# Kernel optimization log

Measured on AMD Instinct MI355X. Metric: run time of the kernel, lower is better.

Reference implementation:

```python
import jax, jax.numpy as jnp
import numpy as np

D = 64            # number of devices (leaves hold D/8 each)
B = 65536         # batch of states
FEAT = 5 + 4 * D  # 261
HID = 128


def setup_inputs() -> dict:
    key = jax.random.key(0)
    ks = jax.random.split(key, 10)
    def nrm(k, shape, s=0.1):
        return jax.random.normal(k, shape, jnp.float32) * s
    return {
        "x": jax.random.normal(ks[0], (B, FEAT), jnp.float32),
        # gate params per depth d: 2^d nodes, weight dim 5 + 4*D/2^d
        "w0": nrm(ks[1], (1, 5 + 4 * D)),
        "b0": jnp.zeros((1,), jnp.float32),
        "w1": nrm(ks[2], (2, 5 + 4 * (D // 2))),
        "b1": jnp.zeros((2,), jnp.float32),
        "w2": nrm(ks[3], (4, 5 + 4 * (D // 4))),
        "b2": jnp.zeros((4,), jnp.float32),
        # leaf prob_dist (torch inits to zeros; random here for a non-trivial baseline)
        "leaf_probs": nrm(ks[4], (8, D // 8), 1.0),
        # critic MLP
        "Wc1": nrm(ks[5], (FEAT, HID)),
        "bc1": jnp.zeros((HID,), jnp.float32),
        "Wc2": nrm(ks[6], (HID, 1)),
        "bc2": jnp.zeros((1,), jnp.float32),
    }


def reference(x, w0, b0, w1, b1, w2, b2, leaf_probs, Wc1, bc1, Wc2, bc2):
    # Batched deterministic ClusterTree routing (exploration disabled).
    x5 = x[:, :5]                       # (B, 5) global features
    dev = x[:, 5:].reshape(B, D, 4)     # (B, D, 4) per-device features
    node = jnp.zeros((B,), jnp.int32)   # current node index at each depth
    cum = jnp.ones((B,), x.dtype)       # product of gate values along path
    for d, (wd, bd) in enumerate([(w0, b0), (w1, b1), (w2, b2)]):
        nd = D >> d                     # devices per node at this depth
        off = node * nd                 # contiguous-cluster start offset
        idx = off[:, None] + jnp.arange(nd)                     # (B, nd)
        dslice = jnp.take_along_axis(dev, idx[:, :, None], 1)   # (B, nd, 4)
        w = wd[node]                    # (B, 5 + 4*nd)
        gate = (jnp.sum(x5 * w[:, :5], -1)
                + jnp.sum(dslice.reshape(B, -1) * w[:, 5:], -1)
                + bd[node])
        val = jax.nn.sigmoid(gate)
        cum = cum * val                 # torch: val * child_output, recursively
        node = node * 2 + (val >= 0.5).astype(jnp.int32)
    p = cum[:, None] * leaf_probs[node]                 # (B, D//8)
    v = jax.nn.relu(x @ Wc1 + bc1) @ Wc2 + bc2          # (B, 1) critic
    return p, v
```

## Files before the change

### kernel.cpp

```cpp
#include <hip/hip_runtime.h>
#include <hip/hip_bf16.h>
#include <stdint.h>

#define NB    65536
#define FEATN 261
#define HIDN  128
#define NSTEP 17
#define SROW  296

#define ROWSF 64
#define NTHRF 256

typedef __attribute__((ext_vector_type(8)))  short bf16x8;
typedef __attribute__((ext_vector_type(16))) float f32x16;
typedef float f32x4u __attribute__((ext_vector_type(4), aligned(4)));

#define MFMA32(A, B, C) __builtin_amdgcn_mfma_f32_32x32x16_bf16(A, B, C, 0, 0, 0)

__device__ __forceinline__ uint16_t f2b(float v) {
    __hip_bfloat16 b = __float2bfloat16(v);
    return *reinterpret_cast<uint16_t*>(&b);
}

__global__ void prep_kernel(const float* __restrict__ Wc1,
                            uint16_t* __restrict__ wsB)
{
    int t = blockIdx.x * 256 + threadIdx.x;
    if (t < NSTEP * 4 * 64) {
        int p = t >> 6, l = t & 63;
        int s = p >> 2, nt = p & 3;
        int n = nt * 32 + (l & 31);
        int kb = 16 * s + 8 * (l >> 5);
        uint16_t hw[8];
        #pragma unroll
        for (int j = 0; j < 8; ++j) {
            int k = kb + j;
            float v = (k < FEATN) ? Wc1[(size_t)k * HIDN + n] : 0.f;
            hw[j] = f2b(v);
        }
        *reinterpret_cast<uint4*>(wsB + (size_t)p * 512 + l * 8) =
            *reinterpret_cast<uint4*>(hw);
    }
}

__global__ __launch_bounds__(NTHRF, 4) void fused_kernel(
    const float* __restrict__ x,
    const float* __restrict__ w0, const float* __restrict__ b0,
    const float* __restrict__ w1, const float* __restrict__ b1,
    const float* __restrict__ w2, const float* __restrict__ b2,
    const float* __restrict__ leaf,
    const uint16_t* __restrict__ wsB,
    const float* __restrict__ bc1, const float* __restrict__ Wc2,
    const float* __restrict__ bc2,
    float* __restrict__ out_p, float* __restrict__ out_v)
{
    __shared__ uint16_t Axs[ROWSF * SROW];
    __shared__ float bc1s[HIDN];
    __shared__ float wc2s[HIDN];
    __shared__ float vpart[ROWSF * 2];

    const int tid = threadIdx.x;
    const int rowBase = blockIdx.x * ROWSF;

    if (tid < HIDN) { bc1s[tid] = bc1[tid]; wc2s[tid] = Wc2[tid]; }
    if (tid < ROWSF) {
        uint16_t* rp = Axs + tid * SROW;
        rp[261] = 0;
        *reinterpret_cast<uint32_t*>(rp + 262) = 0u;
        uint4 z; z.x = z.y = z.z = z.w = 0u;
        *reinterpret_cast<uint4*>(rp + 264) = z;
        *reinterpret_cast<uint4*>(rp + 272) = z;
        *reinterpret_cast<uint4*>(rp + 280) = z;
        *reinterpret_cast<uint4*>(rp + 288) = z;
    }

    for (int idx = tid; idx < ROWSF * 66; idx += NTHRF) {
        int row = idx / 66;
        int seg = idx - row * 66;
        const float* src = x + (size_t)(rowBase + row) * FEATN + 4 * seg;
        uint16_t* dst = Axs + row * SROW + 4 * seg;
        if (seg < 65) {
            f32x4u v = *reinterpret_cast<const f32x4u*>(src);
            uint32_t p0 = (uint32_t)f2b(v[0]) | ((uint32_t)f2b(v[1]) << 16);
            uint32_t p1 = (uint32_t)f2b(v[2]) | ((uint32_t)f2b(v[3]) << 16);
            uint2 pk; pk.x = p0; pk.y = p1;
            *reinterpret_cast<uint2*>(dst) = pk;
        } else {
            dst[0] = f2b(src[0]);
        }
    }

    {
        const int s = tid & 15;
        const int g = tid >> 4;

        f32x4u w0q[4];
        #pragma unroll
        for (int j = 0; j < 4; ++j)
            w0q[j] = *reinterpret_cast<const f32x4u*>(w0 + 4 * s + 64 * j);
        const float w0t = (s < 5) ? w0[256 + s] : 0.f;

        f32x4u w1aq[2], w1bq[2];
        #pragma unroll
        for (int j = 0; j < 2; ++j) {
            w1aq[j] = *reinterpret_cast<const f32x4u*>(w1 + 5 + 8 * s + 4 * j);
            w1bq[j] = *reinterpret_cast<const f32x4u*>(w1 + 133 + 5 + 8 * s + 4 * j);
        }
        const float w1a5 = (s < 5) ? w1[s]       : 0.f;
        const float w1b5 = (s < 5) ? w1[133 + s] : 0.f;

        f32x4u w2q0 = *reinterpret_cast<const f32x4u*>(w2 +  0 * 69 + 5 + 4 * s);
        f32x4u w2q1 = *reinterpret_cast<const f32x4u*>(w2 +  1 * 69 + 5 + 4 * s);
        f32x4u w2q2 = *reinterpret_cast<const f32x4u*>(w2 +  2 * 69 + 5 + 4 * s);
        f32x4u w2q3 = *reinterpret_cast<const f32x4u*>(w2 +  3 * 69 + 5 + 4 * s);
        const float w25_0 = (s < 5) ? w2[0 * 69 + s] : 0.f;
        const float w25_1 = (s < 5) ? w2[1 * 69 + s] : 0.f;
        const float w25_2 = (s < 5) ? w2[2 * 69 + s] : 0.f;
        const float w25_3 = (s < 5) ? w2[3 * 69 + s] : 0.f;

        #pragma unroll 1
        for (int r4 = 0; r4 < 4; ++r4) {
            const int row = rowBase + r4 * 16 + g;
            const float* xr = x + (size_t)row * FEATN;

            f32x4u xq[4];
            #pragma unroll
            for (int j = 0; j < 4; ++j)
                xq[j] = *reinterpret_cast<const f32x4u*>(xr + 4 * s + 64 * j);
            const float xt  = (s < 5) ? xr[256 + s] : 0.f;
            const float xs5 = (s < 5) ? xr[s]       : 0.f;

            float part = xt * w0t;
            #pragma unroll
            for (int j = 0; j < 4; ++j)
                #pragma unroll
                for (int c = 0; c < 4; ++c)
                    part += xq[j][c] * w0q[j][c];
            part += __shfl_xor(part, 1);
            part += __shfl_xor(part, 2);
            part += __shfl_xor(part, 4);
            part += __shfl_xor(part, 8);
            float gate = part + b0[0];
            int node = (gate >= 0.f) ? 1 : 0;
            float cum = 1.f / (1.f + __expf(-gate));

            {
                const float* base = xr + 5 + 128 * node + 8 * s;
                f32x4u xw0 = *reinterpret_cast<const f32x4u*>(base);
                f32x4u xw1 = *reinterpret_cast<const f32x4u*>(base + 4);
                part = xs5 * (node ? w1b5 : w1a5);
                #pragma unroll
                for (int c = 0; c < 4; ++c) {
                    part += xw0[c] * (node ? w1bq[0][c] : w1aq[0][c]);
                    part += xw1[c] * (node ? w1bq[1][c] : w1aq[1][c]);
                }
                part += __shfl_xor(part, 1);
                part += __shfl_xor(part, 2);
                part += __shfl_xor(part, 4);
                part += __shfl_xor(part, 8);
                gate = part + b1[node];
                cum *= 1.f / (1.f + __expf(-gate));
                node = node * 2 + ((gate >= 0.f) ? 1 : 0);
            }
            {
                f32x4u xv2 = *reinterpret_cast<const f32x4u*>(xr + 5 + 64 * node + 4 * s);
                f32x4u t0 = (node & 1) ? w2q1 : w2q0;
                f32x4u t1 = (node & 1) ? w2q3 : w2q2;
                f32x4u wsel = (node & 2) ? t1 : t0;
                float w5a = (node & 1) ? w25_1 : w25_0;
                float w5b = (node & 1) ? w25_3 : w25_2;
                float w5sel = (node & 2) ? w5b : w5a;
                part = xs5 * w5sel;
                #pragma unroll
                for (int c = 0; c < 4; ++c) part += xv2[c] * wsel[c];
                part += __shfl_xor(part, 1);
                part += __shfl_xor(part, 2);
                part += __shfl_xor(part, 4);
                part += __shfl_xor(part, 8);
                gate = part + b2[node];
                cum *= 1.f / (1.f + __expf(-gate));
                node = node * 2 + ((gate >= 0.f) ? 1 : 0);
            }
            if (s < 8)
                out_p[(size_t)row * 8 + s] = cum * leaf[node * 8 + s];
        }
    }

    __syncthreads();

    const int lane = tid & 63;
    const int w    = tid >> 6;
    const int mt   = w >> 1;
    const int nh   = w & 1;

    const uint16_t* arow = Axs + (mt * 32 + (lane & 31)) * SROW + (lane >> 5) * 8;
    const uint16_t* bgl  = wsB + (size_t)(2 * nh) * 512 + lane * 8;

    f32x16 acc0 = {}, acc1 = {};
    #pragma unroll
    for (int ss = 0; ss < NSTEP; ++ss) {
        bf16x8 af  = *reinterpret_cast<const bf16x8*>(arow + ss * 16);
        bf16x8 bf0 = *reinterpret_cast<const bf16x8*>(bgl + (size_t)(ss * 4)     * 512);
        bf16x8 bf1 = *reinterpret_cast<const bf16x8*>(bgl + (size_t)(ss * 4 + 1) * 512);
        acc0 = MFMA32(af, bf0, acc0);
        acc1 = MFMA32(af, bf1, acc1);
    }

    {
        const int c = lane & 31;
        const int q = lane >> 5;
        const int n0 = 2 * nh * 32 + c;
        const int n1 = n0 + 32;
        const float bb0 = bc1s[n0], ww0 = wc2s[n0];
        const float bb1 = bc1s[n1], ww1 = wc2s[n1];

        float pv[16];
        #pragma unroll
        for (int reg = 0; reg < 16; ++reg) {
            float h0 = acc0[reg] + bb0; h0 = h0 > 0.f ? h0 : 0.f;
            float h1 = acc1[reg] + bb1; h1 = h1 > 0.f ? h1 : 0.f;
            float t = h0 * ww0 + h1 * ww1;
            t += __shfl_xor(t, 1);
            t += __shfl_xor(t, 2);
            t += __shfl_xor(t, 4);
            t += __shfl_xor(t, 8);
            t += __shfl_xor(t, 16);
            pv[reg] = t;
        }
        #pragma unroll
        for (int reg = 0; reg < 16; ++reg) {
            if (c == reg) {
                int row_local = (reg & 3) + 8 * (reg >> 2) + 4 * q;
                vpart[(mt * 32 + row_local) * 2 + nh] = pv[reg];
            }
        }
    }
    __syncthreads();
    if (tid < ROWSF)
        out_v[rowBase + tid] = vpart[tid * 2] + vpart[tid * 2 + 1] + bc2[0];
}

extern "C" void kernel_launch(void* const* d_in, const int* in_sizes, int n_in,
                              void* d_out, int out_size, void* d_ws, size_t ws_size,
                              hipStream_t stream) {
    const float* x    = (const float*)d_in[0];
    const float* w0   = (const float*)d_in[1];
    const float* b0   = (const float*)d_in[2];
    const float* w1   = (const float*)d_in[3];
    const float* b1   = (const float*)d_in[4];
    const float* w2   = (const float*)d_in[5];
    const float* b2   = (const float*)d_in[6];
    const float* leaf = (const float*)d_in[7];
    const float* Wc1  = (const float*)d_in[8];
    const float* bc1  = (const float*)d_in[9];
    const float* Wc2  = (const float*)d_in[10];
    const float* bc2  = (const float*)d_in[11];

    uint16_t* wsB = (uint16_t*)d_ws;

    float* out_p = (float*)d_out;
    float* out_v = out_p + (size_t)NB * 8;

    prep_kernel<<<17, 256, 0, stream>>>(Wc1, wsB);
    fused_kernel<<<NB / ROWSF, NTHRF, 0, stream>>>(
        x, w0, b0, w1, b1, w2, b2, leaf, wsB, bc1, Wc2, bc2, out_p, out_v);
}
```

Baseline: 147.0 us.

## Fuse x staging into routing loop and precompute all gate partials speculatively

The separate pass that loads x and converts it to bf16 in shared memory is removed; the routing loop now writes the bf16 row into shared memory from the x registers it already loaded, so x is read from global memory once instead of twice. The gate partial sums for every node at every depth are computed from that single load using rearranged weight registers. The data-dependent reloads of x at depths 1 and 2 are replaced by selecting among the precomputed partials. This removes dependent global loads from the routing chain, at the cost of extra FMAs and a few more weight registers.

Result: faster. 128.0 us, median of 2 (-12.9%).

```diff
diff --git a/kernel.cpp b/kernel.cpp
--- a/kernel.cpp
+++ b/kernel.cpp
@@ -21,6 +21,13 @@
     __hip_bfloat16 b = __float2bfloat16(v);
     return *reinterpret_cast<uint16_t*>(&b);
 }
+
+__device__ __forceinline__ float sigmoidf(float g) {
+    return 1.f / (1.f + __expf(-g));
+}
+
+#define RED16(v) do { v += __shfl_xor(v, 1); v += __shfl_xor(v, 2); \
+                      v += __shfl_xor(v, 4); v += __shfl_xor(v, 8); } while (0)
 
 __global__ void prep_kernel(const float* __restrict__ Wc1,
                             uint16_t* __restrict__ wsB)
@@ -74,116 +81,116 @@
         *reinterpret_cast<uint4*>(rp + 288) = z;
     }
 
-    for (int idx = tid; idx < ROWSF * 66; idx += NTHRF) {
-        int row = idx / 66;
-        int seg = idx - row * 66;
-        const float* src = x + (size_t)(rowBase + row) * FEATN + 4 * seg;
-        uint16_t* dst = Axs + row * SROW + 4 * seg;
-        if (seg < 65) {
-            f32x4u v = *reinterpret_cast<const f32x4u*>(src);
-            uint32_t p0 = (uint32_t)f2b(v[0]) | ((uint32_t)f2b(v[1]) << 16);
-            uint32_t p1 = (uint32_t)f2b(v[2]) | ((uint32_t)f2b(v[3]) << 16);
-            uint2 pk; pk.x = p0; pk.y = p1;
-            *reinterpret_cast<uint2*>(dst) = pk;
-        } else {
-            dst[0] = f2b(src[0]);
-        }
-    }
-
-    {
-        const int s = tid & 15;
-        const int g = tid >> 4;
-
-        f32x4u w0q[4];
+    const int s = tid & 15;
+    const int g = tid >> 4;
+
+    f32x4u w0q[4];
+    #pragma unroll
+    for (int j = 0; j < 4; ++j)
+        w0q[j] = *reinterpret_cast<const f32x4u*>(w0 + 64 * j + 4 * s);
+    const float w0t = (s < 5) ? w0[256 + s] : 0.f;
+
+    float w1v[4][4], w2v[4][4];
+    #pragma unroll
+    for (int j = 0; j < 4; ++j)
+        #pragma unroll
+        for (int c = 0; c < 4; ++c) {
+            int e = 64 * j + 4 * s + c;
+            w1v[j][c] = w1[(e < 133) ? e : e + 5];
+            int n2 = (e < 5) ? 0 : ((e - 5) >> 6);
+            w2v[j][c] = w2[e + 5 * n2];
+        }
+    const float w1t = (s < 5) ? w1[261 + s] : 0.f;
+    const float w2t = (s < 5) ? w2[271 + s] : 0.f;
+
+    const float xw1b  = (s < 5) ? w1[133 + s] : 0.f;
+    const float xw2_1 = (s < 5) ? w2[ 69 + s] : 0.f;
+    const float xw2_2 = (s < 5) ? w2[138 + s] : 0.f;
+    const float xw2_3 = (s < 5) ? w2[207 + s] : 0.f;
+
+    const float b0s  = b0[0];
+    const float b1s0 = b1[0], b1s1 = b1[1];
+    const float b2s0 = b2[0], b2s1 = b2[1], b2s2 = b2[2], b2s3 = b2[3];
+
+    #pragma unroll 1
+    for (int r4 = 0; r4 < 4; ++r4) {
+        const int rl  = r4 * 16 + g;
+        const int row = rowBase + rl;
+        const float* xr = x + (size_t)row * FEATN;
+
+        f32x4u xq[4];
         #pragma unroll
         for (int j = 0; j < 4; ++j)
-            w0q[j] = *reinterpret_cast<const f32x4u*>(w0 + 4 * s + 64 * j);
-        const float w0t = (s < 5) ? w0[256 + s] : 0.f;
-
-        f32x4u w1aq[2], w1bq[2];
-        #pragma unroll
-        for (int j = 0; j < 2; ++j) {
-            w1aq[j] = *reinterpret_cast<const f32x4u*>(w1 + 5 + 8 * s + 4 * j);
-            w1bq[j] = *reinterpret_cast<const f32x4u*>(w1 + 133 + 5 + 8 * s + 4 * j);
-        }
-        const float w1a5 = (s < 5) ? w1[s]       : 0.f;
-        const float w1b5 = (s < 5) ? w1[133 + s] : 0.f;
-
-        f32x4u w2q0 = *reinterpret_cast<const f32x4u*>(w2 +  0 * 69 + 5 + 4 * s);
-        f32x4u w2q1 = *reinterpret_cast<const f32x4u*>(w2 +  1 * 69 + 5 + 4 * s);
-        f32x4u w2q2 = *reinterpret_cast<const f32x4u*>(w2 +  2 * 69 + 5 + 4 * s);
-        f32x4u w2q3 = *reinterpret_cast<const f32x4u*>(w2 +  3 * 69 + 5 + 4 * s);
-        const float w25_0 = (s < 5) ? w2[0 * 69 + s] : 0.f;
-        const float w25_1 = (s < 5) ? w2[1 * 69 + s] : 0.f;
-        const float w25_2 = (s < 5) ? w2[2 * 69 + s] : 0.f;
-        const float w25_3 = (s < 5) ? w2[3 * 69 + s] : 0.f;
-
-        #pragma unroll 1
-        for (int r4 = 0; r4 < 4; ++r4) {
-            const int row = rowBase + r4 * 16 + g;
-            const float* xr = x + (size_t)row * FEATN;
-
-            f32x4u xq[4];
+            xq[j] = *reinterpret_cast<const f32x4u*>(xr + 64 * j + 4 * s);
+        const float xt  = (s < 5) ? xr[256 + s] : 0.f;
+        const float xs5 = (s < 5) ? xr[s]       : 0.f;
+
+        {
+            uint16_t* rp = Axs + rl * SROW;
             #pragma unroll
-            for (int j = 0; j < 4; ++j)
-                xq[j] = *reinterpret_cast<const f32x4u*>(xr + 4 * s + 64 * j);
-            const float xt  = (s < 5) ? xr[256 + s] : 0.f;
-            const float xs5 = (s < 5) ? xr[s]       : 0.f;
-
-            float part = xt * w0t;
+            for (int j = 0; j < 4; ++j) {
+                uint32_t p0w = (uint32_t)f2b(xq[j][0]) | ((uint32_t)f2b(xq[j][1]) << 16);
+                uint32_t p1w = (uint32_t)f2b(xq[j][2]) | ((uint32_t)f2b(xq[j][3]) << 16);
+                uint2 pk; pk.x = p0w; pk.y = p1w;
+                *reinterpret_cast<uint2*>(rp + 64 * j + 4 * s) = pk;
+            }
+            if (s < 5) rp[256 + s] = f2b(xt);
+        }
+
+        float p0 = 0.f, p1a = 0.f, p1b = 0.f;
+        float p2_0 = 0.f, p2_1 = 0.f, p2_2 = 0.f, p2_3 = 0.f;
+        #pragma unroll
+        for (int j = 0; j < 4; ++j)
             #pragma unroll
-            for (int j = 0; j < 4; ++j)
-                #pragma unroll
-                for (int c = 0; c < 4; ++c)
-                    part += xq[j][c] * w0q[j][c];
-            part += __shfl_xor(part, 1);
-            part += __shfl_xor(part, 2);
-            part += __shfl_xor(part, 4);
-            part += __shfl_xor(part, 8);
-            float gate = part + b0[0];
-            int node = (gate >= 0.f) ? 1 : 0;
-            float cum = 1.f / (1.f + __expf(-gate));
-
-            {
-                const float* base = xr + 5 + 128 * node + 8 * s;
-                f32x4u xw0 = *reinterpret_cast<const f32x4u*>(base);
-                f32x4u xw1 = *reinterpret_cast<const f32x4u*>(base + 4);
-                part = xs5 * (node ? w1b5 : w1a5);
-                #pragma unroll
-                for (int c = 0; c < 4; ++c) {
-                    part += xw0[c] * (node ? w1bq[0][c] : w1aq[0][c]);
-                    part += xw1[c] * (node ? w1bq[1][c] : w1aq[1][c]);
+            for (int c = 0; c < 4; ++c) {
+                const float xv = xq[j][c];
+                const bool lo = (4 * s + c) < 5;
+                p0 += xv * w0q[j][c];
+                const float t1 = xv * w1v[j][c];
+                const float t2 = xv * w2v[j][c];
+                if (j == 0) {
+                    p1a += t1;
+                    p2_0 += t2;
+                } else if (j == 1) {
+                    p1a += t1;
+                    p2_0 += lo ? t2 : 0.f;  p2_1 += lo ? 0.f : t2;
+                } else if (j == 2) {
+                    p1a += lo ? t1 : 0.f;   p1b += lo ? 0.f : t1;
+                    p2_1 += lo ? t2 : 0.f;  p2_2 += lo ? 0.f : t2;
+                } else {
+                    p1b += t1;
+                    p2_2 += lo ? t2 : 0.f;  p2_3 += lo ? 0.f : t2;
                 }
-                part += __shfl_xor(part, 1);
-                part += __shfl_xor(part, 2);
-                part += __shfl_xor(part, 4);
-                part += __shfl_xor(part, 8);
-                gate = part + b1[node];
-                cum *= 1.f / (1.f + __expf(-gate));
-                node = node * 2 + ((gate >= 0.f) ? 1 : 0);
             }
-            {
-                f32x4u xv2 = *reinterpret_cast<const f32x4u*>(xr + 5 + 64 * node + 4 * s);
-                f32x4u t0 = (node & 1) ? w2q1 : w2q0;
-                f32x4u t1 = (node & 1) ? w2q3 : w2q2;
-                f32x4u wsel = (node & 2) ? t1 : t0;
-                float w5a = (node & 1) ? w25_1 : w25_0;
-                float w5b = (node & 1) ? w25_3 : w25_2;
-                float w5sel = (node & 2) ? w5b : w5a;
-                part = xs5 * w5sel;
-                #pragma unroll
-                for (int c = 0; c < 4; ++c) part += xv2[c] * wsel[c];
-                part += __shfl_xor(part, 1);
-                part += __shfl_xor(part, 2);
-                part += __shfl_xor(part, 4);
-                part += __shfl_xor(part, 8);
-                gate = part + b2[node];
-                cum *= 1.f / (1.f + __expf(-gate));
-                node = node * 2 + ((gate >= 0.f) ? 1 : 0);
-            }
-            if (s < 8)
-                out_p[(size_t)row * 8 + s] = cum * leaf[node * 8 + s];
-        }
+        p0   += xt * w0t;
+        p1b  += xt * w1t;
+        p2_3 += xt * w2t;
+        p1b  += xs5 * xw1b;
+        p2_1 += xs5 * xw2_1;
+        p2_2 += xs5 * xw2_2;
+        p2_3 += xs5 * xw2_3;
+
+        RED16(p0);
+        const float gate0 = p0 + b0s;
+        int nn = (gate0 >= 0.f) ? 1 : 0;
+        float cum = sigmoidf(gate0);
+
+        float p1 = nn ? p1b : p1a;
+        RED16(p1);
+        const float gate1 = p1 + (nn ? b1s1 : b1s0);
+        nn = nn * 2 + ((gate1 >= 0.f) ? 1 : 0);
+        cum *= sigmoidf(gate1);
+
+        float p2 = (nn & 2) ? ((nn & 1) ? p2_3 : p2_2)
+                            : ((nn & 1) ? p2_1 : p2_0);
+        RED16(p2);
+        const float gate2 = p2 + ((nn & 2) ? ((nn & 1) ? b2s3 : b2s2)
+                                           : ((nn & 1) ? b2s1 : b2s0));
+        nn = nn * 2 + ((gate2 >= 0.f) ? 1 : 0);
+        cum *= sigmoidf(gate2);
+
+        if (s < 8)
+            out_p[(size_t)row * 8 + s] = cum * leaf[nn * 8 + s];
     }
 
     __syncthreads();
```
